# Optimization experiments

Hardware: AMD Instinct MI355X
Metric: run time of the kernel (lower is better)

Reference implementation:

```python
import jax, jax.numpy as jnp
import numpy as np
import math

B, S, D = 2, 2048, 1024
H, DK, DV = 16, 64, 64  # head_count, query_size, value_size; H*DV == D
NEG_INF = -jnp.inf


def setup_inputs() -> dict:
    key = jax.random.key(0)
    ks = jax.random.split(key, 10)
    sc = 0.02
    return {
        "input": jax.random.normal(ks[0], (B, S, D), dtype=jnp.float32),
        "padding_mask": jnp.zeros((B, S), dtype=jnp.float32),  # 0 = valid, 1 = padded
        "wq_w": jax.random.normal(ks[1], (H * DK, D), dtype=jnp.float32) * sc,
        "wq_b": jnp.zeros((H * DK,), dtype=jnp.float32),
        "wk_w": jax.random.normal(ks[2], (H * DK, D), dtype=jnp.float32) * sc,
        "wk_b": jnp.zeros((H * DK,), dtype=jnp.float32),
        "wv_w": jax.random.normal(ks[3], (H * DV, D), dtype=jnp.float32) * sc,
        "wv_b": jnp.zeros((H * DV,), dtype=jnp.float32),
        "fin_w": jax.random.normal(ks[4], (D, H * DV), dtype=jnp.float32) * sc,
        "fin_b": jnp.zeros((D,), dtype=jnp.float32),
    }


def reference(input, padding_mask, wq_w, wq_b, wk_w, wk_b, wv_w, wv_b, fin_w, fin_b):
    b, s, _ = input.shape
    # projections -> [b, h, s, d]
    Q = (input @ wq_w.T + wq_b).reshape(b, s, H, DK).transpose(0, 2, 1, 3)
    K = (input @ wk_w.T + wk_b).reshape(b, s, H, DK).transpose(0, 2, 1, 3)
    V = (input @ wv_w.T + wv_b).reshape(b, s, H, DV).transpose(0, 2, 1, 3)

    # padding mask: pad*(-inf), nan_to_num(0*inf -> 0); broadcast over query dim
    pad = jnp.where(padding_mask > 0, NEG_INF, 0.0)[:, None, None, :]  # [b,1,1,s]
    i = jnp.arange(s)
    causal = jnp.where(i[None, :] < i[:, None] + 1, 0.0, NEG_INF)  # [s,s]
    mask = pad + causal[None, None, :, :]

    # (QK^T + mask) / sqrt(dk), softmax over keys
    logits = (jnp.einsum("bhqd,bhkd->bhqk", Q, K) + mask) / math.sqrt(DK)
    attn = jax.nn.softmax(logits, axis=-1)
    out = jnp.einsum("bhqk,bhkd->bqhd", attn, V).reshape(b, s, H * DV)
    return out @ fin_w.T + fin_b
```

## Files before the change

### kernel.cpp

```cpp
#include <hip/hip_runtime.h>


typedef __bf16 bf16;
typedef __bf16 bf16x4 __attribute__((ext_vector_type(4)));
typedef __bf16 bf16x8 __attribute__((ext_vector_type(8)));
typedef float  f32x4  __attribute__((ext_vector_type(4)));

#define B_  2
#define S_  2048
#define D_  1024
#define H_  16
#define HD  64
#define NEG_BIG (-3.0e38f)
#define SCALE_LOG2E 0.1803368801111204f

#define NSPLIT_QT 14
#define SLOTS_PER_BH (2 * NSPLIT_QT)

__device__ __forceinline__ void lds16(const void* g, void* l) {
    __builtin_amdgcn_global_load_lds((const __attribute__((address_space(1))) void*)g,
                                     (__attribute__((address_space(3))) void*)l, 16, 0, 0);
}

__device__ __forceinline__ f32x4 mfma16(bf16x8 a, bf16x8 b, f32x4 c) {
    return __builtin_amdgcn_mfma_f32_16x16x32_bf16(a, b, c, 0, 0, 0);
}

#define IT(qt, k0, ke) ((uint32_t)(qt) | ((uint32_t)(k0) << 8) | ((uint32_t)(ke) << 16))
__device__ __constant__ uint32_t g_items[46] = {
    IT(16,0,9),  IT(17,0,9),
    IT(30,0,8),  IT(30,8,16), IT(31,0,8),  IT(31,8,16),
    IT(28,0,8),  IT(29,0,8),  IT(14,0,8),  IT(15,0,8),
    IT(28,8,15), IT(29,8,15), IT(26,0,7),  IT(26,7,14),
    IT(27,0,7),  IT(27,7,14), IT(24,0,7),  IT(25,0,7),
    IT(12,0,7),  IT(13,0,7),
    IT(24,7,13), IT(25,7,13), IT(22,0,6),  IT(22,6,12),
    IT(23,0,6),  IT(23,6,12), IT(20,0,6),  IT(21,0,6),
    IT(10,0,6),  IT(11,0,6),
    IT(20,6,11), IT(21,6,11), IT(18,0,5),  IT(18,5,10),
    IT(19,0,5),  IT(19,5,10), IT(8,0,5),   IT(9,0,5),
    IT(6,0,4),   IT(7,0,4),
    IT(4,0,3),   IT(5,0,3),
    IT(2,0,2),   IT(3,0,2),
    IT(0,0,1),   IT(1,0,1)
};

__global__ __launch_bounds__(256) void convert_k(const float* __restrict__ X,
                                                 const float* __restrict__ wq,
                                                 const float* __restrict__ wk,
                                                 const float* __restrict__ wv,
                                                 const float* __restrict__ wo,
                                                 const float* __restrict__ pm,
                                                 bf16* __restrict__ dst,
                                                 bf16* __restrict__ validB) {
    const int gid = blockIdx.x * 256 + threadIdx.x;
    const int i   = gid * 4;
    const float* src;
    int off;
    if      (i < (4 << 20)) { src = X;  off = 0; }
    else if (i < (5 << 20)) { src = wq; off = 4 << 20; }
    else if (i < (6 << 20)) { src = wk; off = 5 << 20; }
    else if (i < (7 << 20)) { src = wv; off = 6 << 20; }
    else                    { src = wo; off = 7 << 20; }
    const float4 v = *(const float4*)(src + (i - off));
    bf16x4 p;
    p[0] = (bf16)v.x; p[1] = (bf16)v.y; p[2] = (bf16)v.z; p[3] = (bf16)v.w;
    *(bf16x4*)(dst + i) = p;
    if (gid < (B_ * S_) / 4) {
        const float4 m = *(const float4*)(pm + gid * 4);
        bf16x4 q;
        q[0] = (bf16)((m.x > 0.f) ? 0.f : 1.f);
        q[1] = (bf16)((m.y > 0.f) ? 0.f : 1.f);
        q[2] = (bf16)((m.z > 0.f) ? 0.f : 1.f);
        q[3] = (bf16)((m.w > 0.f) ? 0.f : 1.f);
        *(bf16x4*)(validB + gid * 4) = q;
    }
}

__global__ __launch_bounds__(256) void gemm_qkv(const bf16* __restrict__ A,
                                                const bf16* __restrict__ Wq,
                                                const bf16* __restrict__ Wk,
                                                const bf16* __restrict__ Wv,
                                                const float* __restrict__ bq,
                                                const float* __restrict__ bk,
                                                const float* __restrict__ bv,
                                                const float* __restrict__ pm,
                                                bf16* __restrict__ Qw,
                                                bf16* __restrict__ Kw,
                                                bf16* __restrict__ Vw) {
    constexpr int K = 1024;
    __shared__ bf16 sA[2][128 * 32];
    __shared__ bf16 sB[2][128 * 32];
    const int tid  = threadIdx.x;
    const int l15  = tid & 15;
    const int quad = (tid & 63) >> 4;
    const int wid  = tid >> 6;
    const int seg  = blockIdx.x >> 3;
    const int bn   = blockIdx.x & 7;
    const int bm   = blockIdx.y;
    const int wm   = (wid >> 1) * 64;
    const int wn   = (wid & 1) * 64;

    const bf16* W    = (seg == 0) ? Wq : (seg == 1) ? Wk : Wv;
    const float* bias = (seg == 0) ? bq : (seg == 1) ? bk : bv;

    const bf16* Ab = A + (size_t)bm * 128 * K;
    const bf16* Wb = W + (size_t)bn * 128 * K;

    f32x4 acc[4][4] = {};
    const int rq = (quad ^ ((l15 >> 1) & 3)) * 8;

#define QSTAGE(BUF, K0) do {                                                    \
    _Pragma("unroll")                                                           \
    for (int it_ = 0; it_ < 2; ++it_) {                                         \
        int c_ = it_ * 256 + tid;                                               \
        int row_ = c_ >> 2, c8_ = c_ & 3;                                       \
        int sw_ = c8_ ^ ((row_ >> 1) & 3);                                      \
        lds16(Ab + row_ * K + (K0) + sw_ * 8, (char*)sA[BUF] + c_ * 16);        \
        lds16(Wb + row_ * K + (K0) + sw_ * 8, (char*)sB[BUF] + c_ * 16);        \
    } } while (0)

    QSTAGE(0, 0);
    __syncthreads();
    int cur = 0;
    for (int k0 = 0; k0 < K; k0 += 32) {
        if (k0 + 32 < K) QSTAGE(cur ^ 1, k0 + 32);
        bf16x8 af[4], bfr[4];
        #pragma unroll
        for (int i = 0; i < 4; ++i)
            af[i] = *(const bf16x8*)&sA[cur][(wm + i * 16 + l15) * 32 + rq];
        #pragma unroll
        for (int i = 0; i < 4; ++i)
            bfr[i] = *(const bf16x8*)&sB[cur][(wn + i * 16 + l15) * 32 + rq];
        #pragma unroll
        for (int mi = 0; mi < 4; ++mi)
            #pragma unroll
            for (int ni = 0; ni < 4; ++ni)
                acc[mi][ni] = mfma16(af[mi], bfr[ni], acc[mi][ni]);
        __syncthreads();
        cur ^= 1;
    }
#undef QSTAGE

    #pragma unroll
    for (int ni = 0; ni < 4; ++ni) {
        const int n  = bn * 128 + wn + ni * 16 + l15;
        const float bv_ = bias[n];
        const int h = n >> 6;
        #pragma unroll
        for (int mi = 0; mi < 4; ++mi) {
            const int m0 = bm * 128 + wm + mi * 16 + quad * 4;
            if (seg == 2) {
                const int dv = n & 63;
                const int b = m0 >> 11, s = m0 & 2047;
                const float4 pmv = *(const float4*)&pm[b * S_ + s];
                bf16x4 pack;
                #pragma unroll
                for (int r = 0; r < 4; ++r) {
                    const float vm = (((const float*)&pmv)[r] > 0.f) ? 0.f : 1.f;
                    pack[r] = (bf16)((acc[mi][ni][r] + bv_) * vm);
                }
                *(bf16x4*)&Vw[(((size_t)(b * H_ + h) * HD + dv) << 11) + s] = pack;
            } else {
                bf16* C = (seg == 0) ? Qw : Kw;
                const float qs = (seg == 0) ? SCALE_LOG2E : 1.0f;
                const int dk = n & 63;
                #pragma unroll
                for (int r = 0; r < 4; ++r) {
                    const int m = m0 + r, b = m >> 11, s = m & 2047;
                    C[(((size_t)(b * H_ + h) << 11) + s) * HD + dk] =
                        (bf16)((acc[mi][ni][r] + bv_) * qs);
                }
            }
        }
    }
}

__global__ __launch_bounds__(256) void gemm_fin(const bf16* __restrict__ A,
                                                const bf16* __restrict__ W,
                                                const float* __restrict__ bias,
                                                float* __restrict__ C) {
    constexpr int N = 1024, K = 1024;
    __shared__ bf16 sA[2][64 * 32];
    __shared__ bf16 sB[2][128 * 32];
    const int tid  = threadIdx.x;
    const int l15  = tid & 15;
    const int quad = (tid & 63) >> 4;
    const int wid  = tid >> 6;
    const int bm   = blockIdx.x >> 3;
    const int bn   = blockIdx.x & 7;
    const int wm   = (wid & 1) * 32;
    const int wn   = (wid >> 1) * 64;

    const bf16* Ab = A + (size_t)bm * 64 * K;
    const bf16* Wb = W + (size_t)bn * 128 * K;

    f32x4 acc[2][4] = {};
    const int rq = (quad ^ ((l15 >> 1) & 3)) * 8;

#define FSTAGE(BUF, K0) do {                                                    \
    {   int c_ = tid;                                                           \
        int row_ = c_ >> 2, c8_ = c_ & 3;                                       \
        int sw_ = c8_ ^ ((row_ >> 1) & 3);                                      \
        lds16(Ab + row_ * K + (K0) + sw_ * 8, (char*)sA[BUF] + c_ * 16); }      \
    _Pragma("unroll")                                                           \
    for (int it_ = 0; it_ < 2; ++it_) {                                         \
        int c_ = it_ * 256 + tid;                                               \
        int row_ = c_ >> 2, c8_ = c_ & 3;                                       \
        int sw_ = c8_ ^ ((row_ >> 1) & 3);                                      \
        lds16(Wb + row_ * K + (K0) + sw_ * 8, (char*)sB[BUF] + c_ * 16);        \
    } } while (0)

    FSTAGE(0, 0);
    __syncthreads();
    int cur = 0;
    for (int k0 = 0; k0 < K; k0 += 32) {
        if (k0 + 32 < K) FSTAGE(cur ^ 1, k0 + 32);
        bf16x8 af[2], bfr[4];
        #pragma unroll
        for (int i = 0; i < 2; ++i)
            af[i] = *(const bf16x8*)&sA[cur][(wm + i * 16 + l15) * 32 + rq];
        #pragma unroll
        for (int i = 0; i < 4; ++i)
            bfr[i] = *(const bf16x8*)&sB[cur][(wn + i * 16 + l15) * 32 + rq];
        #pragma unroll
        for (int mi = 0; mi < 2; ++mi)
            #pragma unroll
            for (int ni = 0; ni < 4; ++ni)
                acc[mi][ni] = mfma16(af[mi], bfr[ni], acc[mi][ni]);
        __syncthreads();
        cur ^= 1;
    }
#undef FSTAGE

    #pragma unroll
    for (int ni = 0; ni < 4; ++ni) {
        const int n  = bn * 128 + wn + ni * 16 + l15;
        const float bv = bias[n];
        #pragma unroll
        for (int mi = 0; mi < 2; ++mi) {
            const int m0 = bm * 64 + wm + mi * 16 + quad * 4;
            #pragma unroll
            for (int r = 0; r < 4; ++r)
                C[(size_t)(m0 + r) * N + n] = acc[mi][ni][r] + bv;
        }
    }
}

__global__ __launch_bounds__(256, 4) void attn_k(const bf16* __restrict__ Q,
                                                 const bf16* __restrict__ K,
                                                 const bf16* __restrict__ Vt,
                                                 const bf16* __restrict__ validB,
                                                 float* __restrict__ Opart,
                                                 float* __restrict__ Lpart,
                                                 bf16* __restrict__ Aout) {
    __shared__ bf16 sK_[2 * 128 * 32];
    __shared__ bf16 sV[4 * 64 * 32];
    const int tid  = threadIdx.x;
    const int l15  = tid & 15;
    const int quad = (tid & 63) >> 4;
    const int wid  = tid >> 6;
    const int bh   = blockIdx.x & 31;
    const int b    = bh >> 4;
    const int h    = bh & 15;

    const uint32_t itm = g_items[blockIdx.x >> 5];
    const int qt  = itm & 255;
    const int kt0 = (itm >> 8) & 255;
    const int kte = (itm >> 16) & 255;
    const int nkt = (qt >> 1) + 1;
    const bool split = (qt >= 18);

    const bf16* Qg = Q  + (size_t)bh * S_ * HD;
    const bf16* Kg = K  + (size_t)bh * S_ * HD;
    const bf16* Vg = Vt + (size_t)bh * HD * S_;
    const bf16* vB = validB + b * S_;

    bf16x8 qb[2];
    #pragma unroll
    for (int kk = 0; kk < 2; ++kk)
        qb[kk] = *(const bf16x8*)&Qg[(qt * 64 + wid * 16 + l15) * HD + kk * 32 + quad * 8];

    const int krow0 = (l15 >> 2) * 8 + (l15 & 3);
    const int qg    = qt * 64 + wid * 16 + l15;
    const int ckx = (quad ^ (((l15 >> 1) & 1) | (((l15 >> 2) & 1) << 1))) * 8;
    const int cvx = (quad ^ (((l15 >> 1) & 1) | (((l15 >> 3) & 1) << 1))) * 8;

    f32x4 o[4]  = {};
    f32x4 lacc  = {};

    for (int kt = kt0; kt < kte; ++kt) {
        __syncthreads();
        #pragma unroll
        for (int it = 0; it < 4; ++it) {
            int c = it * 256 + tid;
            { int pl = c >> 9, row = (c >> 2) & 127, c8 = c & 3;
              int sw = c8 ^ (((row >> 1) & 1) | (((row >> 3) & 1) << 1));
              lds16(Kg + ((size_t)kt * 128 + row) * HD + pl * 32 + sw * 8,
                    (char*)sK_ + c * 16); }
            { int kc = c >> 8, dv = (c >> 2) & 63, c8 = c & 3;
              int sw = c8 ^ (((dv >> 1) & 1) | (((dv >> 3) & 1) << 1));
              lds16(Vg + (size_t)kt * 128 + (size_t)dv * S_ + kc * 32 + sw * 8,
                    (char*)sV + c * 16); }
        }
        bf16x8 vf[4];
        #pragma unroll
        for (int g = 0; g < 4; ++g)
            vf[g] = *(const bf16x8*)&vB[kt * 128 + g * 32 + quad * 8];
        __syncthreads();

        const bool lastt = (kt == nkt - 1);
        #pragma unroll
        for (int g = 0; g < 4; ++g) {
            f32x4 s[2] = {};
            #pragma unroll
            for (int f = 0; f < 2; ++f)
                #pragma unroll
                for (int kk = 0; kk < 2; ++kk) {
                    bf16x8 ka = *(const bf16x8*)
                        &sK_[(kk * 128 + g * 32 + krow0 + f * 4) * 32 + ckx];
                    s[f] = mfma16(ka, qb[kk], s[f]);
                }
            bf16x8 pb;
            #pragma unroll
            for (int f = 0; f < 2; ++f)
                #pragma unroll
                for (int r = 0; r < 4; ++r) {
                    float v = s[f][r];
                    if (lastt && (kt * 128 + g * 32 + quad * 8 + f * 4 + r > qg))
                        v = NEG_BIG;
                    pb[f * 4 + r] = (bf16)exp2f(v);
                }
            lacc = mfma16(vf[g], pb, lacc);
            #pragma unroll
            for (int dvf = 0; dvf < 4; ++dvf) {
                bf16x8 va = *(const bf16x8*)
                    &sV[(g * 64 + dvf * 16 + l15) * 32 + cvx];
                o[dvf] = mfma16(va, pb, o[dvf]);
            }
        }
    }

    if (split) {
        const int sidx = (qt - 18) * 2 + (kt0 ? 1 : 0);
        const int slot = bh * SLOTS_PER_BH + sidx;
        const int q    = wid * 16 + l15;
        float* Ob = Opart + ((size_t)slot << 12) + q * 64 + quad * 4;
        #pragma unroll
        for (int dvf = 0; dvf < 4; ++dvf)
            *(f32x4*)(Ob + dvf * 16) = o[dvf];
        if (quad == 0) Lpart[slot * 64 + q] = lacc[0];
    } else {
        const float inv = 1.f / lacc[0];
        const size_t base = ((size_t)b * S_ + qg) * D_ + h * HD + quad * 4;
        #pragma unroll
        for (int dvf = 0; dvf < 4; ++dvf) {
            bf16x4 pk;
            #pragma unroll
            for (int r = 0; r < 4; ++r) pk[r] = (bf16)(o[dvf][r] * inv);
            *(bf16x4*)&Aout[base + dvf * 16] = pk;
        }
    }
}

__global__ __launch_bounds__(256) void combine_k(const float* __restrict__ Opart,
                                                 const float* __restrict__ Lpart,
                                                 bf16* __restrict__ Aw) {
    const int gid  = blockIdx.x * 256 + threadIdx.x;
    const int dc   = gid & 7;
    const int q    = (gid >> 3) & 63;
    const int rest = gid >> 9;
    const int qth  = rest % NSPLIT_QT;
    const int bh   = rest / NSPLIT_QT;
    const int slot0 = bh * SLOTS_PER_BH + qth * 2;
    const float l = Lpart[slot0 * 64 + q] + Lpart[(slot0 + 1) * 64 + q];
    const float inv = 1.f / l;
    const float* O0 = Opart + ((size_t)slot0 << 12) + q * 64 + dc * 8;
    const float* O1 = O0 + 4096;
    const float4 a0 = *(const float4*)O0;
    const float4 a1 = *(const float4*)(O0 + 4);
    const float4 b0 = *(const float4*)O1;
    const float4 b1 = *(const float4*)(O1 + 4);
    bf16x8 p;
    p[0] = (bf16)((a0.x + b0.x) * inv); p[1] = (bf16)((a0.y + b0.y) * inv);
    p[2] = (bf16)((a0.z + b0.z) * inv); p[3] = (bf16)((a0.w + b0.w) * inv);
    p[4] = (bf16)((a1.x + b1.x) * inv); p[5] = (bf16)((a1.y + b1.y) * inv);
    p[6] = (bf16)((a1.z + b1.z) * inv); p[7] = (bf16)((a1.w + b1.w) * inv);
    const int b = bh >> 4, h = bh & 15;
    const int s = (18 + qth) * 64 + q;
    *(bf16x8*)&Aw[((size_t)(b * S_ + s)) * D_ + h * HD + dc * 8] = p;
}

extern "C" void kernel_launch(void* const* d_in, const int* in_sizes, int n_in,
                              void* d_out, int out_size, void* d_ws, size_t ws_size,
                              hipStream_t stream) {
    const float* X   = (const float*)d_in[0];
    const float* pm  = (const float*)d_in[1];
    const float* wq  = (const float*)d_in[2];
    const float* bq  = (const float*)d_in[3];
    const float* wk  = (const float*)d_in[4];
    const float* bk  = (const float*)d_in[5];
    const float* wv  = (const float*)d_in[6];
    const float* bvb = (const float*)d_in[7];
    const float* wo  = (const float*)d_in[8];
    const float* bo  = (const float*)d_in[9];
    float* out = (float*)d_out;

    char* ws = (char*)d_ws;
    bf16* Xb  = (bf16*)(ws);
    bf16* Wqb = (bf16*)(ws + (8u  << 20));
    bf16* Wkb = (bf16*)(ws + (10u << 20));
    bf16* Wvb = (bf16*)(ws + (12u << 20));
    bf16* Wob = (bf16*)(ws + (14u << 20));
    bf16* Qw  = (bf16*)(ws + (16u << 20));
    bf16* Kw  = (bf16*)(ws + (24u << 20));
    bf16* Vw  = (bf16*)(ws + (32u << 20));
    bf16* Aw  = (bf16*)(ws + (40u << 20));
    float* Opart = (float*)(ws);
    bf16*  validB = (bf16*)(ws + (48u << 20));
    float* Lpart  = (float*)(ws + (48u << 20) + 65536);

    convert_k<<<dim3(8192), dim3(256), 0, stream>>>(X, wq, wk, wv, wo, pm,
                                                    Xb, validB);
    gemm_qkv<<<dim3(24, 32), dim3(256), 0, stream>>>(Xb, Wqb, Wkb, Wvb,
                                                     bq, bk, bvb, pm,
                                                     Qw, Kw, Vw);
    attn_k<<<dim3(1472), dim3(256), 0, stream>>>(Qw, Kw, Vw, validB,
                                                 Opart, Lpart, Aw);
    combine_k<<<dim3(896), dim3(256), 0, stream>>>(Opart, Lpart, Aw);
    gemm_fin<<<dim3(512), dim3(256), 0, stream>>>(Aw, Wob, bo, out);
}
```

Baseline: 197.9 us.

## Fuse fp32-to-bf16 conversion into GEMMs and split-combine into output projection

Drops the standalone conversion kernel: both GEMMs now load fp32 inputs and weights into registers and convert them to bf16 while writing to shared memory, replacing the async global-to-LDS loads. The valid-mask conversion moves into one block of the QKV GEMM. The combine kernel is also removed: the final GEMM reads the split partial outputs and normalisers directly for rows in the split region and normalises them on the fly. This saves two launches and the intermediate bf16 round trips, but doubles global read bytes per tile, costs register staging, and makes the split rows' normalisation repeat per N-block.

```diff
diff --git a/kernel.cpp b/kernel.cpp
--- a/kernel.cpp
+++ b/kernel.cpp
@@ -24,6 +24,13 @@
 
 __device__ __forceinline__ f32x4 mfma16(bf16x8 a, bf16x8 b, f32x4 c) {
     return __builtin_amdgcn_mfma_f32_16x16x32_bf16(a, b, c, 0, 0, 0);
+}
+
+__device__ __forceinline__ bf16x8 cvt8(const float4 a, const float4 b) {
+    bf16x8 v;
+    v[0] = (bf16)a.x; v[1] = (bf16)a.y; v[2] = (bf16)a.z; v[3] = (bf16)a.w;
+    v[4] = (bf16)b.x; v[5] = (bf16)b.y; v[6] = (bf16)b.z; v[7] = (bf16)b.w;
+    return v;
 }
 
 #define IT(qt, k0, ke) ((uint32_t)(qt) | ((uint32_t)(k0) << 8) | ((uint32_t)(ke) << 16))
@@ -45,49 +52,18 @@
     IT(0,0,1),   IT(1,0,1)
 };
 
-__global__ __launch_bounds__(256) void convert_k(const float* __restrict__ X,
-                                                 const float* __restrict__ wq,
-                                                 const float* __restrict__ wk,
-                                                 const float* __restrict__ wv,
-                                                 const float* __restrict__ wo,
-                                                 const float* __restrict__ pm,
-                                                 bf16* __restrict__ dst,
-                                                 bf16* __restrict__ validB) {
-    const int gid = blockIdx.x * 256 + threadIdx.x;
-    const int i   = gid * 4;
-    const float* src;
-    int off;
-    if      (i < (4 << 20)) { src = X;  off = 0; }
-    else if (i < (5 << 20)) { src = wq; off = 4 << 20; }
-    else if (i < (6 << 20)) { src = wk; off = 5 << 20; }
-    else if (i < (7 << 20)) { src = wv; off = 6 << 20; }
-    else                    { src = wo; off = 7 << 20; }
-    const float4 v = *(const float4*)(src + (i - off));
-    bf16x4 p;
-    p[0] = (bf16)v.x; p[1] = (bf16)v.y; p[2] = (bf16)v.z; p[3] = (bf16)v.w;
-    *(bf16x4*)(dst + i) = p;
-    if (gid < (B_ * S_) / 4) {
-        const float4 m = *(const float4*)(pm + gid * 4);
-        bf16x4 q;
-        q[0] = (bf16)((m.x > 0.f) ? 0.f : 1.f);
-        q[1] = (bf16)((m.y > 0.f) ? 0.f : 1.f);
-        q[2] = (bf16)((m.z > 0.f) ? 0.f : 1.f);
-        q[3] = (bf16)((m.w > 0.f) ? 0.f : 1.f);
-        *(bf16x4*)(validB + gid * 4) = q;
-    }
-}
-
-__global__ __launch_bounds__(256) void gemm_qkv(const bf16* __restrict__ A,
-                                                const bf16* __restrict__ Wq,
-                                                const bf16* __restrict__ Wk,
-                                                const bf16* __restrict__ Wv,
+__global__ __launch_bounds__(256) void gemm_qkv(const float* __restrict__ X,
+                                                const float* __restrict__ Wqf,
+                                                const float* __restrict__ Wkf,
+                                                const float* __restrict__ Wvf,
                                                 const float* __restrict__ bq,
                                                 const float* __restrict__ bk,
                                                 const float* __restrict__ bv,
                                                 const float* __restrict__ pm,
                                                 bf16* __restrict__ Qw,
                                                 bf16* __restrict__ Kw,
-                                                bf16* __restrict__ Vw) {
+                                                bf16* __restrict__ Vw,
+                                                bf16* __restrict__ validB) {
     constexpr int K = 1024;
     __shared__ bf16 sA[2][128 * 32];
     __shared__ bf16 sB[2][128 * 32];
@@ -101,30 +77,58 @@
     const int wm   = (wid >> 1) * 64;
     const int wn   = (wid & 1) * 64;
 
-    const bf16* W    = (seg == 0) ? Wq : (seg == 1) ? Wk : Wv;
-    const float* bias = (seg == 0) ? bq : (seg == 1) ? bk : bv;
-
-    const bf16* Ab = A + (size_t)bm * 128 * K;
-    const bf16* Wb = W + (size_t)bn * 128 * K;
+    if (blockIdx.x == 0 && blockIdx.y == 0) {
+        #pragma unroll
+        for (int i = 0; i < 4; ++i) {
+            const int idx = (i * 256 + tid) * 4;
+            const float4 m = *(const float4*)&pm[idx];
+            bf16x4 q;
+            q[0] = (bf16)((m.x > 0.f) ? 0.f : 1.f);
+            q[1] = (bf16)((m.y > 0.f) ? 0.f : 1.f);
+            q[2] = (bf16)((m.z > 0.f) ? 0.f : 1.f);
+            q[3] = (bf16)((m.w > 0.f) ? 0.f : 1.f);
+            *(bf16x4*)&validB[idx] = q;
+        }
+    }
+
+    const float* Wf   = (seg == 0) ? Wqf : (seg == 1) ? Wkf : Wvf;
+    const float* bias = (seg == 0) ? bq  : (seg == 1) ? bk  : bv;
+
+    const float* Ab = X  + (size_t)bm * 128 * K;
+    const float* Wb = Wf + (size_t)bn * 128 * K;
 
     f32x4 acc[4][4] = {};
     const int rq = (quad ^ ((l15 >> 1) & 3)) * 8;
 
-#define QSTAGE(BUF, K0) do {                                                    \
+    float4 rA[2][2], rW[2][2];
+
+#define QLOAD(K0) do {                                                          \
     _Pragma("unroll")                                                           \
     for (int it_ = 0; it_ < 2; ++it_) {                                         \
         int c_ = it_ * 256 + tid;                                               \
         int row_ = c_ >> 2, c8_ = c_ & 3;                                       \
         int sw_ = c8_ ^ ((row_ >> 1) & 3);                                      \
-        lds16(Ab + row_ * K + (K0) + sw_ * 8, (char*)sA[BUF] + c_ * 16);        \
-        lds16(Wb + row_ * K + (K0) + sw_ * 8, (char*)sB[BUF] + c_ * 16);        \
+        const float* pA_ = Ab + (size_t)row_ * K + (K0) + sw_ * 8;              \
+        rA[it_][0] = *(const float4*)pA_;                                       \
+        rA[it_][1] = *(const float4*)(pA_ + 4);                                 \
+        const float* pW_ = Wb + (size_t)row_ * K + (K0) + sw_ * 8;              \
+        rW[it_][0] = *(const float4*)pW_;                                       \
+        rW[it_][1] = *(const float4*)(pW_ + 4);                                 \
     } } while (0)
 
-    QSTAGE(0, 0);
+#define QWRITE(BUF) do {                                                        \
+    _Pragma("unroll")                                                           \
+    for (int it_ = 0; it_ < 2; ++it_) {                                         \
+        int c_ = it_ * 256 + tid;                                               \
+        *(bf16x8*)((char*)sA[BUF] + c_ * 16) = cvt8(rA[it_][0], rA[it_][1]);    \
+        *(bf16x8*)((char*)sB[BUF] + c_ * 16) = cvt8(rW[it_][0], rW[it_][1]);    \
+    } } while (0)
+
+    QLOAD(0); QWRITE(0);
     __syncthreads();
     int cur = 0;
     for (int k0 = 0; k0 < K; k0 += 32) {
-        if (k0 + 32 < K) QSTAGE(cur ^ 1, k0 + 32);
+        if (k0 + 32 < K) QLOAD(k0 + 32);
         bf16x8 af[4], bfr[4];
         #pragma unroll
         for (int i = 0; i < 4; ++i)
@@ -137,10 +141,12 @@
             #pragma unroll
             for (int ni = 0; ni < 4; ++ni)
                 acc[mi][ni] = mfma16(af[mi], bfr[ni], acc[mi][ni]);
+        if (k0 + 32 < K) QWRITE(cur ^ 1);
         __syncthreads();
         cur ^= 1;
     }
-#undef QSTAGE
+#undef QLOAD
+#undef QWRITE
 
     #pragma unroll
     for (int ni = 0; ni < 4; ++ni) {
@@ -176,77 +182,6 @@
     }
 }
 
-__global__ __launch_bounds__(256) void gemm_fin(const bf16* __restrict__ A,
-                                                const bf16* __restrict__ W,
-                                                const float* __restrict__ bias,
-                                                float* __restrict__ C) {
-    constexpr int N = 1024, K = 1024;
-    __shared__ bf16 sA[2][64 * 32];
-    __shared__ bf16 sB[2][128 * 32];
-    const int tid  = threadIdx.x;
-    const int l15  = tid & 15;
-    const int quad = (tid & 63) >> 4;
-    const int wid  = tid >> 6;
-    const int bm   = blockIdx.x >> 3;
-    const int bn   = blockIdx.x & 7;
-    const int wm   = (wid & 1) * 32;
-    const int wn   = (wid >> 1) * 64;
-
-    const bf16* Ab = A + (size_t)bm * 64 * K;
-    const bf16* Wb = W + (size_t)bn * 128 * K;
-
-    f32x4 acc[2][4] = {};
-    const int rq = (quad ^ ((l15 >> 1) & 3)) * 8;
-
-#define FSTAGE(BUF, K0) do {                                                    \
-    {   int c_ = tid;                                                           \
-        int row_ = c_ >> 2, c8_ = c_ & 3;                                       \
-        int sw_ = c8_ ^ ((row_ >> 1) & 3);                                      \
-        lds16(Ab + row_ * K + (K0) + sw_ * 8, (char*)sA[BUF] + c_ * 16); }      \
-    _Pragma("unroll")                                                           \
-    for (int it_ = 0; it_ < 2; ++it_) {                                         \
-        int c_ = it_ * 256 + tid;                                               \
-        int row_ = c_ >> 2, c8_ = c_ & 3;                                       \
-        int sw_ = c8_ ^ ((row_ >> 1) & 3);                                      \
-        lds16(Wb + row_ * K + (K0) + sw_ * 8, (char*)sB[BUF] + c_ * 16);        \
-    } } while (0)
-
-    FSTAGE(0, 0);
-    __syncthreads();
-    int cur = 0;
-    for (int k0 = 0; k0 < K; k0 += 32) {
-        if (k0 + 32 < K) FSTAGE(cur ^ 1, k0 + 32);
-        bf16x8 af[2], bfr[4];
-        #pragma unroll
-        for (int i = 0; i < 2; ++i)
-            af[i] = *(const bf16x8*)&sA[cur][(wm + i * 16 + l15) * 32 + rq];
-        #pragma unroll
-        for (int i = 0; i < 4; ++i)
-            bfr[i] = *(const bf16x8*)&sB[cur][(wn + i * 16 + l15) * 32 + rq];
-        #pragma unroll
-        for (int mi = 0; mi < 2; ++mi)
-            #pragma unroll
-            for (int ni = 0; ni < 4; ++ni)
-                acc[mi][ni] = mfma16(af[mi], bfr[ni], acc[mi][ni]);
-        __syncthreads();
-        cur ^= 1;
-    }
-#undef FSTAGE
-
-    #pragma unroll
-    for (int ni = 0; ni < 4; ++ni) {
-        const int n  = bn * 128 + wn + ni * 16 + l15;
-        const float bv = bias[n];
-        #pragma unroll
-        for (int mi = 0; mi < 2; ++mi) {
-            const int m0 = bm * 64 + wm + mi * 16 + quad * 4;
-            #pragma unroll
-            for (int r = 0; r < 4; ++r)
-                C[(size_t)(m0 + r) * N + n] = acc[mi][ni][r] + bv;
-        }
-    }
-}
-
 __global__ __launch_bounds__(256, 4) void attn_k(const bf16* __restrict__ Q,
                                                  const bf16* __restrict__ K,
                                                  const bf16* __restrict__ Vt,
@@ -363,32 +298,136 @@
     }
 }
 
-__global__ __launch_bounds__(256) void combine_k(const float* __restrict__ Opart,
-                                                 const float* __restrict__ Lpart,
-                                                 bf16* __restrict__ Aw) {
-    const int gid  = blockIdx.x * 256 + threadIdx.x;
-    const int dc   = gid & 7;
-    const int q    = (gid >> 3) & 63;
-    const int rest = gid >> 9;
-    const int qth  = rest % NSPLIT_QT;
-    const int bh   = rest / NSPLIT_QT;
-    const int slot0 = bh * SLOTS_PER_BH + qth * 2;
-    const float l = Lpart[slot0 * 64 + q] + Lpart[(slot0 + 1) * 64 + q];
-    const float inv = 1.f / l;
-    const float* O0 = Opart + ((size_t)slot0 << 12) + q * 64 + dc * 8;
-    const float* O1 = O0 + 4096;
-    const float4 a0 = *(const float4*)O0;
-    const float4 a1 = *(const float4*)(O0 + 4);
-    const float4 b0 = *(const float4*)O1;
-    const float4 b1 = *(const float4*)(O1 + 4);
-    bf16x8 p;
-    p[0] = (bf16)((a0.x + b0.x) * inv); p[1] = (bf16)((a0.y + b0.y) * inv);
-    p[2] = (bf16)((a0.z + b0.z) * inv); p[3] = (bf16)((a0.w + b0.w) * inv);
-    p[4] = (bf16)((a1.x + b1.x) * inv); p[5] = (bf16)((a1.y + b1.y) * inv);
-    p[6] = (bf16)((a1.z + b1.z) * inv); p[7] = (bf16)((a1.w + b1.w) * inv);
-    const int b = bh >> 4, h = bh & 15;
-    const int s = (18 + qth) * 64 + q;
-    *(bf16x8*)&Aw[((size_t)(b * S_ + s)) * D_ + h * HD + dc * 8] = p;
+__global__ __launch_bounds__(256) void gemm_fin(const bf16* __restrict__ A,
+                                                const float* __restrict__ Wo,
+                                                const float* __restrict__ bias,
+                                                const float* __restrict__ Opart,
+                                                const float* __restrict__ Lpart,
+                                                float* __restrict__ C) {
+    constexpr int N = 1024, K = 1024;
+    __shared__ bf16 sAb[2][64 * 32];
+    __shared__ bf16 sBb[2][128 * 32];
+    const int tid  = threadIdx.x;
+    const int l15  = tid & 15;
+    const int quad = (tid & 63) >> 4;
+    const int wid  = tid >> 6;
+    const int bm   = blockIdx.x >> 3;
+    const int bn   = blockIdx.x & 7;
+    const int wm   = (wid & 1) * 32;
+    const int wn   = (wid >> 1) * 64;
+
+    const bf16*  Ab = A  + (size_t)bm * 64 * K;
+    const float* Wb = Wo + (size_t)bn * 128 * K;
+
+    const bool spl = ((bm * 64) & 2047) >= 1152;
+    const int rowA = tid >> 2, c8A = tid & 3;
+    const int swA  = c8A ^ ((rowA >> 1) & 3);
+    const int mA   = bm * 64 + rowA;
+    const int bA   = mA >> 11, srow = mA & 2047;
+    const int qA   = srow & 63;
+    const int qthA = (srow >> 6) - 18;
+
+    f32x4 acc[2][4] = {};
+    const int rq = (quad ^ ((l15 >> 1) & 3)) * 8;
+
+    float4 rW[2][2], rO[4];
+    float  lA0 = 1.f, lA1 = 0.f;
+
+#define FLOADW(K0) do {                                                         \
+    _Pragma("unroll")                                                           \
+    for (int it_ = 0; it_ < 2; ++it_) {                                         \
+        int c_ = it_ * 256 + tid;                                               \
+        int row_ = c_ >> 2, c8_ = c_ & 3;                                       \
+        int sw_ = c8_ ^ ((row_ >> 1) & 3);                                      \
+        const float* p_ = Wb + (size_t)row_ * K + (K0) + sw_ * 8;               \
+        rW[it_][0] = *(const float4*)p_;                                        \
+        rW[it_][1] = *(const float4*)(p_ + 4);                                  \
+    } } while (0)
+
+#define FWRITEW(BUF) do {                                                       \
+    _Pragma("unroll")                                                           \
+    for (int it_ = 0; it_ < 2; ++it_) {                                         \
+        int c_ = it_ * 256 + tid;                                               \
+        *(bf16x8*)((char*)sBb[BUF] + c_ * 16) = cvt8(rW[it_][0], rW[it_][1]);   \
+    } } while (0)
+
+#define FLOADA(K0) do {                                                         \
+    const int h_ = (K0) >> 6;                                                   \
+    const int dvo_ = ((K0) & 32) + swA * 8;                                     \
+    const int slot0_ = ((bA << 4) + h_) * SLOTS_PER_BH + qthA * 2;              \
+    const float* p_ = Opart + ((size_t)slot0_ << 12) + qA * 64 + dvo_;          \
+    rO[0] = *(const float4*)p_;       rO[1] = *(const float4*)(p_ + 4);         \
+    rO[2] = *(const float4*)(p_ + 4096); rO[3] = *(const float4*)(p_ + 4100);   \
+    lA0 = Lpart[slot0_ * 64 + qA]; lA1 = Lpart[slot0_ * 64 + 64 + qA];          \
+    } while (0)
+
+#define FWRITEA(BUF) do {                                                       \
+    const float inv_ = 1.f / (lA0 + lA1);                                       \
+    bf16x8 v_;                                                                  \
+    v_[0] = (bf16)((rO[0].x + rO[2].x) * inv_);                                 \
+    v_[1] = (bf16)((rO[0].y + rO[2].y) * inv_);                                 \
+    v_[2] = (bf16)((rO[0].z + rO[2].z) * inv_);                                 \
+    v_[3] = (bf16)((rO[0].w + rO[2].w) * inv_);                                 \
+    v_[4] = (bf16)((rO[1].x + rO[3].x) * inv_);                                 \
+    v_[5] = (bf16)((rO[1].y + rO[3].y) * inv_);                                 \
+    v_[6] = (bf16)((rO[1].z + rO[3].z) * inv_);                                 \
+    v_[7] = (bf16)((rO[1].w + rO[3].w) * inv_);                                 \
+    *(bf16x8*)((char*)sAb[BUF] + tid * 16) = v_;                                \
+    } while (0)
+
+#define FLDSA(BUF, K0) do {                                                     \
+    lds16(Ab + (size_t)rowA * K + (K0) + swA * 8,                               \
+          (char*)sAb[BUF] + tid * 16);                                          \
+    } while (0)
+
+    FLOADW(0);
+    if (spl) FLOADA(0); else FLDSA(0, 0);
+    FWRITEW(0);
+    if (spl) FWRITEA(0);
+    __syncthreads();
+    int cur = 0;
+    for (int k0 = 0; k0 < K; k0 += 32) {
+        if (k0 + 32 < K) {
+            FLOADW(k0 + 32);
+            if (spl) FLOADA(k0 + 32); else FLDSA(cur ^ 1, k0 + 32);
+        }
+        bf16x8 af[2], bfr[4];
+        #pragma unroll
+        for (int i = 0; i < 2; ++i)
+            af[i] = *(const bf16x8*)&sAb[cur][(wm + i * 16 + l15) * 32 + rq];
+        #pragma unroll
+        for (int i = 0; i < 4; ++i)
+            bfr[i] = *(const bf16x8*)&sBb[cur][(wn + i * 16 + l15) * 32 + rq];
+        #pragma unroll
+        for (int mi = 0; mi < 2; ++mi)
+            #pragma unroll
+            for (int ni = 0; ni < 4; ++ni)
+                acc[mi][ni] = mfma16(af[mi], bfr[ni], acc[mi][ni]);
+        if (k0 + 32 < K) {
+            FWRITEW(cur ^ 1);
+            if (spl) FWRITEA(cur ^ 1);
+        }
+        __syncthreads();
+        cur ^= 1;
+    }
+#undef FLOADW
+#undef FWRITEW
+#undef FLOADA
+#undef FWRITEA
+#undef FLDSA
+
+    #pragma unroll
+    for (int ni = 0; ni < 4; ++ni) {
+        const int n  = bn * 128 + wn + ni * 16 + l15;
+        const float bv = bias[n];
+        #pragma unroll
+        for (int mi = 0; mi < 2; ++mi) {
+            const int m0 = bm * 64 + wm + mi * 16 + quad * 4;
+            #pragma unroll
+            for (int r = 0; r < 4; ++r)
+                C[(size_t)(m0 + r) * N + n] = acc[mi][ni][r] + bv;
+        }
+    }
 }
 
 extern "C" void kernel_launch(void* const* d_in, const int* in_sizes, int n_in,
@@ -407,26 +446,19 @@
     float* out = (float*)d_out;
 
     char* ws = (char*)d_ws;
-    bf16* Xb  = (bf16*)(ws);
-    bf16* Wqb = (bf16*)(ws + (8u  << 20));
-    bf16* Wkb = (bf16*)(ws + (10u << 20));
-    bf16* Wvb = (bf16*)(ws + (12u << 20));
-    bf16* Wob = (bf16*)(ws + (14u << 20));
-    bf16* Qw  = (bf16*)(ws + (16u << 20));
-    bf16* Kw  = (bf16*)(ws + (24u << 20));
-    bf16* Vw  = (bf16*)(ws + (32u << 20));
-    bf16* Aw  = (bf16*)(ws + (40u << 20));
-    float* Opart = (float*)(ws);
-    bf16*  validB = (bf16*)(ws + (48u << 20));
-    float* Lpart  = (float*)(ws + (48u << 20) + 65536);
-
-    convert_k<<<dim3(8192), dim3(256), 0, stream>>>(X, wq, wk, wv, wo, pm,
-                                                    Xb, validB);
-    gemm_qkv<<<dim3(24, 32), dim3(256), 0, stream>>>(Xb, Wqb, Wkb, Wvb,
+    float* Opart  = (float*)(ws);
+    float* Lpart  = (float*)(ws + (14u << 20));
+    bf16*  validB = (bf16*)(ws + (15u << 20));
+    bf16*  Qw     = (bf16*)(ws + (16u << 20));
+    bf16*  Kw     = (bf16*)(ws + (24u << 20));
+    bf16*  Vw     = (bf16*)(ws + (32u << 20));
+    bf16*  Aw     = (bf16*)(ws + (40u << 20));
+
+    gemm_qkv<<<dim3(24, 32), dim3(256), 0, stream>>>(X, wq, wk, wv,
                                                      bq, bk, bvb, pm,
-                                                     Qw, Kw, Vw);
+                                                     Qw, Kw, Vw, validB);
     attn_k<<<dim3(1472), dim3(256), 0, stream>>>(Qw, Kw, Vw, validB,
                                                  Opart, Lpart, Aw);
-    combine_k<<<dim3(896), dim3(256), 0, stream>>>(Opart, Lpart, Aw);
-    gemm_fin<<<dim3(512), dim3(256), 0, stream>>>(Aw, Wob, bo, out);
-}
+    gemm_fin<<<dim3(512), dim3(256), 0, stream>>>(Aw, wo, bo,
+                                                  Opart, Lpart, out);
+}
```

After: 212.7 us. +7.5%, slower.

## Fuse split-K attention combine into final GEMM A-tile load; widen convert

Applied to the files above, without the earlier changes.

The separate combine kernel is removed. For row tiles whose query positions were split across two attention partials, the final projection GEMM now loads both fp32 partial outputs and the partial sums into registers, normalises and converts them to bf16, and writes them into the shared-memory A tile. Other rows still use the direct global-to-LDS copy. This saves a launch and a round trip of the combined activations through global memory, but the fused path does more register work and serialises part of the load. Separately, the conversion kernel now handles 8 elements per thread with half the blocks.

```diff
diff --git a/kernel.cpp b/kernel.cpp
--- a/kernel.cpp
+++ b/kernel.cpp
@@ -24,6 +24,13 @@
 
 __device__ __forceinline__ f32x4 mfma16(bf16x8 a, bf16x8 b, f32x4 c) {
     return __builtin_amdgcn_mfma_f32_16x16x32_bf16(a, b, c, 0, 0, 0);
+}
+
+__device__ __forceinline__ bf16x8 cvt8(const float4 a, const float4 b) {
+    bf16x8 v;
+    v[0] = (bf16)a.x; v[1] = (bf16)a.y; v[2] = (bf16)a.z; v[3] = (bf16)a.w;
+    v[4] = (bf16)b.x; v[5] = (bf16)b.y; v[6] = (bf16)b.z; v[7] = (bf16)b.w;
+    return v;
 }
 
 #define IT(qt, k0, ke) ((uint32_t)(qt) | ((uint32_t)(k0) << 8) | ((uint32_t)(ke) << 16))
@@ -54,7 +61,7 @@
                                                  bf16* __restrict__ dst,
                                                  bf16* __restrict__ validB) {
     const int gid = blockIdx.x * 256 + threadIdx.x;
-    const int i   = gid * 4;
+    const int i   = gid * 8;
     const float* src;
     int off;
     if      (i < (4 << 20)) { src = X;  off = 0; }
@@ -62,18 +69,22 @@
     else if (i < (6 << 20)) { src = wk; off = 5 << 20; }
     else if (i < (7 << 20)) { src = wv; off = 6 << 20; }
     else                    { src = wo; off = 7 << 20; }
-    const float4 v = *(const float4*)(src + (i - off));
-    bf16x4 p;
-    p[0] = (bf16)v.x; p[1] = (bf16)v.y; p[2] = (bf16)v.z; p[3] = (bf16)v.w;
-    *(bf16x4*)(dst + i) = p;
-    if (gid < (B_ * S_) / 4) {
-        const float4 m = *(const float4*)(pm + gid * 4);
-        bf16x4 q;
-        q[0] = (bf16)((m.x > 0.f) ? 0.f : 1.f);
-        q[1] = (bf16)((m.y > 0.f) ? 0.f : 1.f);
-        q[2] = (bf16)((m.z > 0.f) ? 0.f : 1.f);
-        q[3] = (bf16)((m.w > 0.f) ? 0.f : 1.f);
-        *(bf16x4*)(validB + gid * 4) = q;
+    const float4 v0 = *(const float4*)(src + (i - off));
+    const float4 v1 = *(const float4*)(src + (i - off) + 4);
+    *(bf16x8*)(dst + i) = cvt8(v0, v1);
+    if (gid < (B_ * S_) / 8) {
+        const float4 m0 = *(const float4*)(pm + gid * 8);
+        const float4 m1 = *(const float4*)(pm + gid * 8 + 4);
+        bf16x8 q;
+        q[0] = (bf16)((m0.x > 0.f) ? 0.f : 1.f);
+        q[1] = (bf16)((m0.y > 0.f) ? 0.f : 1.f);
+        q[2] = (bf16)((m0.z > 0.f) ? 0.f : 1.f);
+        q[3] = (bf16)((m0.w > 0.f) ? 0.f : 1.f);
+        q[4] = (bf16)((m1.x > 0.f) ? 0.f : 1.f);
+        q[5] = (bf16)((m1.y > 0.f) ? 0.f : 1.f);
+        q[6] = (bf16)((m1.z > 0.f) ? 0.f : 1.f);
+        q[7] = (bf16)((m1.w > 0.f) ? 0.f : 1.f);
+        *(bf16x8*)(validB + gid * 8) = q;
     }
 }
 
@@ -176,77 +187,6 @@
     }
 }
 
-__global__ __launch_bounds__(256) void gemm_fin(const bf16* __restrict__ A,
-                                                const bf16* __restrict__ W,
-                                                const float* __restrict__ bias,
-                                                float* __restrict__ C) {
-    constexpr int N = 1024, K = 1024;
-    __shared__ bf16 sA[2][64 * 32];
-    __shared__ bf16 sB[2][128 * 32];
-    const int tid  = threadIdx.x;
-    const int l15  = tid & 15;
-    const int quad = (tid & 63) >> 4;
-    const int wid  = tid >> 6;
-    const int bm   = blockIdx.x >> 3;
-    const int bn   = blockIdx.x & 7;
-    const int wm   = (wid & 1) * 32;
-    const int wn   = (wid >> 1) * 64;
-
-    const bf16* Ab = A + (size_t)bm * 64 * K;
-    const bf16* Wb = W + (size_t)bn * 128 * K;
-
-    f32x4 acc[2][4] = {};
-    const int rq = (quad ^ ((l15 >> 1) & 3)) * 8;
-
-#define FSTAGE(BUF, K0) do {                                                    \
-    {   int c_ = tid;                                                           \
-        int row_ = c_ >> 2, c8_ = c_ & 3;                                       \
-        int sw_ = c8_ ^ ((row_ >> 1) & 3);                                      \
-        lds16(Ab + row_ * K + (K0) + sw_ * 8, (char*)sA[BUF] + c_ * 16); }      \
-    _Pragma("unroll")                                                           \
-    for (int it_ = 0; it_ < 2; ++it_) {                                         \
-        int c_ = it_ * 256 + tid;                                               \
-        int row_ = c_ >> 2, c8_ = c_ & 3;                                       \
-        int sw_ = c8_ ^ ((row_ >> 1) & 3);                                      \
-        lds16(Wb + row_ * K + (K0) + sw_ * 8, (char*)sB[BUF] + c_ * 16);        \
-    } } while (0)
-
-    FSTAGE(0, 0);
-    __syncthreads();
-    int cur = 0;
-    for (int k0 = 0; k0 < K; k0 += 32) {
-        if (k0 + 32 < K) FSTAGE(cur ^ 1, k0 + 32);
-        bf16x8 af[2], bfr[4];
-        #pragma unroll
-        for (int i = 0; i < 2; ++i)
-            af[i] = *(const bf16x8*)&sA[cur][(wm + i * 16 + l15) * 32 + rq];
-        #pragma unroll
-        for (int i = 0; i < 4; ++i)
-            bfr[i] = *(const bf16x8*)&sB[cur][(wn + i * 16 + l15) * 32 + rq];
-        #pragma unroll
-        for (int mi = 0; mi < 2; ++mi)
-            #pragma unroll
-            for (int ni = 0; ni < 4; ++ni)
-                acc[mi][ni] = mfma16(af[mi], bfr[ni], acc[mi][ni]);
-        __syncthreads();
-        cur ^= 1;
-    }
-#undef FSTAGE
-
-    #pragma unroll
-    for (int ni = 0; ni < 4; ++ni) {
-        const int n  = bn * 128 + wn + ni * 16 + l15;
-        const float bv = bias[n];
-        #pragma unroll
-        for (int mi = 0; mi < 2; ++mi) {
-            const int m0 = bm * 64 + wm + mi * 16 + quad * 4;
-            #pragma unroll
-            for (int r = 0; r < 4; ++r)
-                C[(size_t)(m0 + r) * N + n] = acc[mi][ni][r] + bv;
-        }
-    }
-}
-
 __global__ __launch_bounds__(256, 4) void attn_k(const bf16* __restrict__ Q,
                                                  const bf16* __restrict__ K,
                                                  const bf16* __restrict__ Vt,
@@ -363,32 +303,121 @@
     }
 }
 
-__global__ __launch_bounds__(256) void combine_k(const float* __restrict__ Opart,
-                                                 const float* __restrict__ Lpart,
-                                                 bf16* __restrict__ Aw) {
-    const int gid  = blockIdx.x * 256 + threadIdx.x;
-    const int dc   = gid & 7;
-    const int q    = (gid >> 3) & 63;
-    const int rest = gid >> 9;
-    const int qth  = rest % NSPLIT_QT;
-    const int bh   = rest / NSPLIT_QT;
-    const int slot0 = bh * SLOTS_PER_BH + qth * 2;
-    const float l = Lpart[slot0 * 64 + q] + Lpart[(slot0 + 1) * 64 + q];
-    const float inv = 1.f / l;
-    const float* O0 = Opart + ((size_t)slot0 << 12) + q * 64 + dc * 8;
-    const float* O1 = O0 + 4096;
-    const float4 a0 = *(const float4*)O0;
-    const float4 a1 = *(const float4*)(O0 + 4);
-    const float4 b0 = *(const float4*)O1;
-    const float4 b1 = *(const float4*)(O1 + 4);
-    bf16x8 p;
-    p[0] = (bf16)((a0.x + b0.x) * inv); p[1] = (bf16)((a0.y + b0.y) * inv);
-    p[2] = (bf16)((a0.z + b0.z) * inv); p[3] = (bf16)((a0.w + b0.w) * inv);
-    p[4] = (bf16)((a1.x + b1.x) * inv); p[5] = (bf16)((a1.y + b1.y) * inv);
-    p[6] = (bf16)((a1.z + b1.z) * inv); p[7] = (bf16)((a1.w + b1.w) * inv);
-    const int b = bh >> 4, h = bh & 15;
-    const int s = (18 + qth) * 64 + q;
-    *(bf16x8*)&Aw[((size_t)(b * S_ + s)) * D_ + h * HD + dc * 8] = p;
+__global__ __launch_bounds__(256) void gemm_fin(const bf16* __restrict__ A,
+                                                const bf16* __restrict__ W,
+                                                const float* __restrict__ bias,
+                                                const float* __restrict__ Opart,
+                                                const float* __restrict__ Lpart,
+                                                float* __restrict__ C) {
+    constexpr int N = 1024, K = 1024;
+    __shared__ bf16 sAb[2][64 * 32];
+    __shared__ bf16 sBb[2][128 * 32];
+    const int tid  = threadIdx.x;
+    const int l15  = tid & 15;
+    const int quad = (tid & 63) >> 4;
+    const int wid  = tid >> 6;
+    const int bm   = blockIdx.x >> 3;
+    const int bn   = blockIdx.x & 7;
+    const int wm   = (wid & 1) * 32;
+    const int wn   = (wid >> 1) * 64;
+
+    const bf16* Ab = A + (size_t)bm * 64 * K;
+    const bf16* Wb = W + (size_t)bn * 128 * K;
+
+    const bool spl = ((bm * 64) & 2047) >= 1152;
+    const int rowA = tid >> 2, c8A = tid & 3;
+    const int swA  = c8A ^ ((rowA >> 1) & 3);
+    const int mA   = bm * 64 + rowA;
+    const int bA   = mA >> 11, srow = mA & 2047;
+    const int qA   = srow & 63;
+    const int qthA = (srow >> 6) - 18;
+
+    f32x4 acc[2][4] = {};
+    const int rq = (quad ^ ((l15 >> 1) & 3)) * 8;
+
+    float4 rO[4];
+    float  lA0 = 1.f, lA1 = 0.f;
+
+#define FSTW(BUF, K0) do {                                                      \
+    _Pragma("unroll")                                                           \
+    for (int it_ = 0; it_ < 2; ++it_) {                                         \
+        int c_ = it_ * 256 + tid;                                               \
+        int row_ = c_ >> 2, c8_ = c_ & 3;                                       \
+        int sw_ = c8_ ^ ((row_ >> 1) & 3);                                      \
+        lds16(Wb + row_ * K + (K0) + sw_ * 8, (char*)sBb[BUF] + c_ * 16);       \
+    } } while (0)
+
+#define FLDSA(BUF, K0) do {                                                     \
+    lds16(Ab + (size_t)rowA * K + (K0) + swA * 8,                               \
+          (char*)sAb[BUF] + tid * 16);                                          \
+    } while (0)
+
+#define FLOADA(K0) do {                                                         \
+    const int h_ = (K0) >> 6;                                                   \
+    const int dvo_ = ((K0) & 32) + swA * 8;                                     \
+    const int slot0_ = ((bA << 4) + h_) * SLOTS_PER_BH + qthA * 2;              \
+    const float* p_ = Opart + ((size_t)slot0_ << 12) + qA * 64 + dvo_;          \
+    rO[0] = *(const float4*)p_;          rO[1] = *(const float4*)(p_ + 4);      \
+    rO[2] = *(const float4*)(p_ + 4096); rO[3] = *(const float4*)(p_ + 4100);   \
+    lA0 = Lpart[slot0_ * 64 + qA]; lA1 = Lpart[slot0_ * 64 + 64 + qA];          \
+    } while (0)
+
+#define FWRITEA(BUF) do {                                                       \
+    const float inv_ = 1.f / (lA0 + lA1);                                       \
+    bf16x8 v_;                                                                  \
+    v_[0] = (bf16)((rO[0].x + rO[2].x) * inv_);                                 \
+    v_[1] = (bf16)((rO[0].y + rO[2].y) * inv_);                                 \
+    v_[2] = (bf16)((rO[0].z + rO[2].z) * inv_);                                 \
+    v_[3] = (bf16)((rO[0].w + rO[2].w) * inv_);                                 \
+    v_[4] = (bf16)((rO[1].x + rO[3].x) * inv_);                                 \
+    v_[5] = (bf16)((rO[1].y + rO[3].y) * inv_);                                 \
+    v_[6] = (bf16)((rO[1].z + rO[3].z) * inv_);                                 \
+    v_[7] = (bf16)((rO[1].w + rO[3].w) * inv_);                                 \
+    *(bf16x8*)((char*)sAb[BUF] + tid * 16) = v_;                                \
+    } while (0)
+
+    FSTW(0, 0);
+    if (spl) { FLOADA(0); FWRITEA(0); } else FLDSA(0, 0);
+    __syncthreads();
+    int cur = 0;
+    for (int k0 = 0; k0 < K; k0 += 32) {
+        if (k0 + 32 < K) {
+            FSTW(cur ^ 1, k0 + 32);
+            if (spl) FLOADA(k0 + 32); else FLDSA(cur ^ 1, k0 + 32);
+        }
+        bf16x8 af[2], bfr[4];
+        #pragma unroll
+        for (int i = 0; i < 2; ++i)
+            af[i] = *(const bf16x8*)&sAb[cur][(wm + i * 16 + l15) * 32 + rq];
+        #pragma unroll
+        for (int i = 0; i < 4; ++i)
+            bfr[i] = *(const bf16x8*)&sBb[cur][(wn + i * 16 + l15) * 32 + rq];
+        #pragma unroll
+        for (int mi = 0; mi < 2; ++mi)
+            #pragma unroll
+            for (int ni = 0; ni < 4; ++ni)
+                acc[mi][ni] = mfma16(af[mi], bfr[ni], acc[mi][ni]);
+        if (k0 + 32 < K && spl) FWRITEA(cur ^ 1);
+        __syncthreads();
+        cur ^= 1;
+    }
+#undef FSTW
+#undef FLDSA
+#undef FLOADA
+#undef FWRITEA
+
+    #pragma unroll
+    for (int ni = 0; ni < 4; ++ni) {
+        const int n  = bn * 128 + wn + ni * 16 + l15;
+        const float bv = bias[n];
+        #pragma unroll
+        for (int mi = 0; mi < 2; ++mi) {
+            const int m0 = bm * 64 + wm + mi * 16 + quad * 4;
+            #pragma unroll
+            for (int r = 0; r < 4; ++r)
+                C[(size_t)(m0 + r) * N + n] = acc[mi][ni][r] + bv;
+        }
+    }
 }
 
 extern "C" void kernel_launch(void* const* d_in, const int* in_sizes, int n_in,
@@ -416,17 +445,17 @@
     bf16* Kw  = (bf16*)(ws + (24u << 20));
     bf16* Vw  = (bf16*)(ws + (32u << 20));
     bf16* Aw  = (bf16*)(ws + (40u << 20));
-    float* Opart = (float*)(ws);
+    float* Opart  = (float*)(ws);
     bf16*  validB = (bf16*)(ws + (48u << 20));
     float* Lpart  = (float*)(ws + (48u << 20) + 65536);
 
-    convert_k<<<dim3(8192), dim3(256), 0, stream>>>(X, wq, wk, wv, wo, pm,
+    convert_k<<<dim3(4096), dim3(256), 0, stream>>>(X, wq, wk, wv, wo, pm,
                                                     Xb, validB);
     gemm_qkv<<<dim3(24, 32), dim3(256), 0, stream>>>(Xb, Wqb, Wkb, Wvb,
                                                      bq, bk, bvb, pm,
                                                      Qw, Kw, Vw);
     attn_k<<<dim3(1472), dim3(256), 0, stream>>>(Qw, Kw, Vw, validB,
                                                  Opart, Lpart, Aw);
-    combine_k<<<dim3(896), dim3(256), 0, stream>>>(Opart, Lpart, Aw);
-    gemm_fin<<<dim3(512), dim3(256), 0, stream>>>(Aw, Wob, bo, out);
-}
+    gemm_fin<<<dim3(512), dim3(256), 0, stream>>>(Aw, Wob, bo,
+                                                  Opart, Lpart, out);
+}
```

After: 199.1 us. Within noise of the previous version (+0.6%).
